# Performance work log

Hardware: AMD Instinct MI355X
Metric: run time of the kernel (lower is better)

## Reference

```python
import jax, jax.numpy as jnp
import numpy as np

# Search geometry (matches init_kwargs)
WS, WT, PS, K, STRIDE0 = 9, 1, 7, 10, 4
SEARCH_INPUT = "noisy"
ALPHA = 0.5
CRIT = "l2"


def _extract_patches(vid, ti, hi, wi):
    """vid: [T,H,W,C]; ti/hi/wi int32 with shape [...] (patch top-left corners).
    Returns [..., PS*PS*C] with clamped (edge-replicated) boundary handling."""
    T, H, W, C = vid.shape
    dy = jnp.arange(PS)
    dx = jnp.arange(PS)
    hh = jnp.clip(hi[..., None, None] + dy[:, None], 0, H - 1)  # [...,PS,1]
    ww = jnp.clip(wi[..., None, None] + dx[None, :], 0, W - 1)  # [...,1,PS]
    p = vid[ti[..., None, None], hh, ww]  # [...,PS,PS,C]
    return p.reshape(p.shape[:-3] + (PS * PS * C,))


def _nls(vid, fflow, bflow):
    """NonLocalSearch: vid [T,H,W,C], flows [T,H,W,2] (channel 0 = x/w, 1 = y/h).
    Returns (topk_dists [nq,K], inds = (ti,hi,wi,tk,hk,wk))."""
    T, H, W, C = vid.shape
    nH, nW = H // STRIDE0, W // STRIDE0
    ti, hi, wi = jnp.meshgrid(jnp.arange(T), jnp.arange(nH) * STRIDE0,
                              jnp.arange(nW) * STRIDE0, indexing="ij")
    ti, hi, wi = ti.reshape(-1), hi.reshape(-1), wi.reshape(-1)  # [nq]
    q = _extract_patches(vid, ti, hi, wi)  # [nq, PS*PS*C]

    ff = fflow[ti, hi, wi]  # [nq,2] flow to frame t+1
    bf = bflow[ti, hi, wi]  # [nq,2] flow to frame t-1
    zero = jnp.zeros_like(ff)
    flow_dt = jnp.stack([bf, zero, ff], axis=1)  # [nq, 2*WT+1, 2] for dt=-1,0,+1
    dts = jnp.arange(-WT, WT + 1)
    tj = jnp.clip(ti[:, None] + dts[None, :], 0, T - 1)  # [nq, 2*WT+1]
    bh = jnp.clip(hi[:, None] + jnp.round(flow_dt[..., 1]).astype(jnp.int32), 0, H - 1)
    bw = jnp.clip(wi[:, None] + jnp.round(flow_dt[..., 0]).astype(jnp.int32), 0, W - 1)

    # Candidate schedule: (dt_index, oy, ox) for all (2*WT+1)*WS*WS candidates.
    r = WS // 2
    oy, ox = np.meshgrid(np.arange(-r, r + 1), np.arange(-r, r + 1), indexing="ij")
    nt = 2 * WT + 1
    specs = np.stack([np.repeat(np.arange(nt), WS * WS),
                      np.tile(oy.ravel(), nt),
                      np.tile(ox.ravel(), nt)], axis=1).astype(np.int32)  # [S,3]

    def step(_, spec):
        di, sy, sx = spec[0], spec[1], spec[2]
        tjc = tj[:, di]
        hj = jnp.clip(bh[:, di] + sy, 0, H - 1)
        wj = jnp.clip(bw[:, di] + sx, 0, W - 1)
        cp = _extract_patches(vid, tjc, hj, wj)  # [nq,D]
        d = jnp.sum((q - cp) ** 2, axis=-1)  # L2 patch distance, [nq]
        return None, (d, tjc, hj, wj)

    _, (dists, tjs, hjs, wjs) = jax.lax.scan(step, None, jnp.asarray(specs))
    # dists: [S, nq] -> top-K smallest per query
    negd, idx = jax.lax.top_k(-dists.T, K)  # [nq,K]
    tk = jnp.take_along_axis(tjs.T, idx, axis=1)
    hk = jnp.take_along_axis(hjs.T, idx, axis=1)
    wk = jnp.take_along_axis(wjs.T, idx, axis=1)
    return -negd, (ti, hi, wi, tk, hk, wk)


def _refine(vid, inds):
    """RefineSearch with wr=1,kr=1: recompute L2 patch distances at given inds."""
    ti, hi, wi, tk, hk, wk = inds
    q = _extract_patches(vid, ti, hi, wi)          # [nq, D]
    cp = _extract_patches(vid, tk, hk, wk)         # [nq, K, D]
    return jnp.sum((q[:, None, :] - cp) ** 2, axis=-1)  # [nq, K]


def setup_inputs() -> dict:
    key = jax.random.key(0)
    k1, k2, k3, k4 = jax.random.split(key, 4)
    B, T, C, H, W = 1, 5, 3, 384, 384
    noisy = jax.random.normal(k1, (B, T, C, H, W), dtype=jnp.float32)
    deno = jax.random.normal(k2, (B, T, C, H, W), dtype=jnp.float32)
    fflow = jax.random.normal(k3, (B, T, 2, H, W), dtype=jnp.float32)
    bflow = jax.random.normal(k4, (B, T, 2, H, W), dtype=jnp.float32)
    return {"noisy": noisy, "deno": deno, "fflow": fflow, "bflow": bflow}


def reference(noisy, deno, fflow, bflow):
    def per_video(nv, dv, ff, bf):
        nv_t = jnp.transpose(nv, (0, 2, 3, 1))  # [T,H,W,C]
        dv_t = jnp.transpose(dv, (0, 2, 3, 1))
        ff_t = jnp.transpose(ff, (0, 2, 3, 1))  # [T,H,W,2]
        bf_t = jnp.transpose(bf, (0, 2, 3, 1))
        if SEARCH_INPUT == "noisy":
            srch = nv_t
        elif SEARCH_INPUT == "deno":
            srch = dv_t
        else:  # interp
            srch = ALPHA * nv_t + (1.0 - ALPHA) * dv_t
        _, inds = _nls(srch, ff_t, bf_t)
        return _refine(nv_t, inds)  # [nq, K]

    dists = jax.vmap(per_video)(noisy, deno, fflow, bflow)  # [B, nq, K]
    if CRIT == "l1":
        return jnp.mean(jnp.sqrt(dists))
    return jnp.mean(dists)
```

## Files before the change

kernel.cpp:

```cpp
#include <hip/hip_runtime.h>

#define TT 5
#define HH 384
#define WW 384
#define CC 3
#define PS_ 7
#define WSR 4
#define NH_ 96
#define NW_ 96
#define NQ_ (TT*NH_*NW_)
#define NCAND 243
#define KK 10

typedef _Float16 h2v __attribute__((ext_vector_type(2)));
union U32H2 { unsigned u; h2v h; };

__global__ __launch_bounds__(256) void nls_kernel(
    const float* __restrict__ vid,
    const float* __restrict__ fflow,
    const float* __restrict__ bflow,
    float* __restrict__ ws)
{
    const int q   = blockIdx.x;
    const int tid = threadIdx.x;
    const int t   = q / (NH_*NW_);
    const int rem = q % (NH_*NW_);
    const int hi  = (rem / NW_) * 4;
    const int wi  = (rem % NW_) * 4;

    __shared__ unsigned reg_lds[2160];
    __shared__ unsigned qp_lds[84];
    __shared__ float dist[256];

    const float ffx = fflow[((t*2+0)*HH + hi)*WW + wi];
    const float ffy = fflow[((t*2+1)*HH + hi)*WW + wi];
    const float bfx = bflow[((t*2+0)*HH + hi)*WW + wi];
    const float bfy = bflow[((t*2+1)*HH + hi)*WW + wi];

    const int tj0 = (t-1 < 0) ? 0 : (t-1);
    const int tj2 = (t+1 > TT-1) ? (TT-1) : (t+1);
    const int bh0 = min(max(hi + (int)rintf(bfy), 0), HH-1);
    const int bw0 = min(max(wi + (int)rintf(bfx), 0), WW-1);
    const int bh2 = min(max(hi + (int)rintf(ffy), 0), HH-1);
    const int bw2 = min(max(wi + (int)rintf(ffx), 0), WW-1);
    const int rm0 = max(bh0-WSR, 0), cm0 = max(bw0-WSR, 0);
    const int rm1 = max(hi -WSR, 0), cm1 = max(wi -WSR, 0);
    const int rm2 = max(bh2-WSR, 0), cm2 = max(bw2-WSR, 0);

    for (int i = tid; i < 2160; i += 256) {
        int d  = i / 720;
        int rr = i % 720;
        int c  = rr / 240;
        int r2 = rr % 240;
        int r  = r2 >> 4;
        int k  = r2 & 15;
        int tjd = (d==0) ? tj0 : ((d==1) ? t   : tj2);
        int rm  = (d==0) ? rm0 : ((d==1) ? rm1 : rm2);
        int cm  = (d==0) ? cm0 : ((d==1) ? cm1 : cm2);
        int col0 = (k < 8) ? (2*k) : (2*(k-8)+1);
        int row  = min(rm + r, HH-1);
        const float* vrow = vid + (size_t)((tjd*CC + c)*HH + row)*WW;
        float v0 = vrow[min(cm+col0,   WW-1)];
        float v1 = vrow[min(cm+col0+1, WW-1)];
        U32H2 u; u.h.x = (_Float16)v0; u.h.y = (_Float16)v1;
        reg_lds[i] = u.u;
    }
    if (tid < 84) {
        int c  = tid / 28;
        int rr = tid % 28;
        int dy = rr >> 2;
        int k  = rr & 3;
        int row = min(hi+dy, HH-1);
        const float* vrow = vid + (size_t)((t*CC + c)*HH + row)*WW;
        float v0 = vrow[min(wi + 2*k, WW-1)];
        float v1 = (k==3) ? 0.0f : vrow[min(wi + 2*k + 1, WW-1)];
        U32H2 u; u.h.x = (_Float16)v0; u.h.y = (_Float16)v1;
        qp_lds[tid] = u.u;
    }
    __syncthreads();

    float acc = 0.0f;
    if (tid < NCAND) {
        int di = tid / 81;
        int s  = tid % 81;
        int sy = s / 9 - WSR;
        int sx = s % 9 - WSR;
        int bhd = (di==0) ? bh0 : ((di==1) ? hi : bh2);
        int bwd = (di==0) ? bw0 : ((di==1) ? wi : bw2);
        int rm  = (di==0) ? rm0 : ((di==1) ? rm1 : rm2);
        int cm  = (di==0) ? cm0 : ((di==1) ? cm1 : cm2);
        int hj = min(max(bhd + sy, 0), HH-1);
        int wj = min(max(bwd + sx, 0), WW-1);
        int roff = hj - rm;
        int woff = wj - cm;
        int par  = woff & 1;
        int cb   = (woff >> 1) + (par << 3);
        const unsigned* rbase = reg_lds + ((di*3*15 + roff)*16 + cb);
        #pragma unroll
        for (int c = 0; c < CC; c++) {
            const unsigned* rc = rbase + c*240;
            #pragma unroll
            for (int dy = 0; dy < PS_; dy++) {
                #pragma unroll
                for (int k = 0; k < 4; k++) {
                    U32H2 a, b, d;
                    a.u = rc[dy*16 + k];
                    b.u = qp_lds[c*28 + dy*4 + k];
                    d.h = a.h - b.h;
                    if (k == 3) d.u &= 0x0000FFFFu;
#if defined(__has_builtin) && __has_builtin(__builtin_amdgcn_fdot2)
                    acc = __builtin_amdgcn_fdot2(d.h, d.h, acc, false);
#else
                    acc += (float)d.h.x*(float)d.h.x + (float)d.h.y*(float)d.h.y;
#endif
                }
            }
        }
    }
    dist[tid] = (tid < NCAND) ? acc : __int_as_float(0x7f800000);
    __syncthreads();

    if (tid < 64) {
        float sumk = 0.0f;
        #pragma unroll 1
        for (int k = 0; k < KK; k++) {
            unsigned key = 0xFFFFFFFFu;
            #pragma unroll
            for (int j = 0; j < 4; j++) {
                int slot = tid + j*64;
                unsigned b = __float_as_uint(dist[slot]);
                unsigned pk = (b & 0xFFFFFF00u) | (unsigned)slot;
                key = min(key, pk);
            }
            #pragma unroll
            for (int ofs = 1; ofs < 64; ofs <<= 1)
                key = min(key, (unsigned)__shfl_xor((int)key, ofs, 64));
            int slot = (int)(key & 0xFFu);
            sumk += dist[slot];
            if (tid == 0) dist[slot] = __int_as_float(0x7f800000);
        }
        if (tid == 0) ws[q] = sumk;
    }
}

__global__ __launch_bounds__(1024) void reduce_kernel(
    const float* __restrict__ ws, float* __restrict__ out)
{
    __shared__ float sdata[1024];
    float s = 0.0f;
    for (int i = threadIdx.x; i < NQ_; i += 1024) s += ws[i];
    sdata[threadIdx.x] = s;
    __syncthreads();
    for (int ofs = 512; ofs > 0; ofs >>= 1) {
        if ((int)threadIdx.x < ofs) sdata[threadIdx.x] += sdata[threadIdx.x + ofs];
        __syncthreads();
    }
    if (threadIdx.x == 0) out[0] = sdata[0] * (1.0f / (float)(NQ_ * KK));
}

extern "C" void kernel_launch(void* const* d_in, const int* in_sizes, int n_in,
                              void* d_out, int out_size, void* d_ws, size_t ws_size,
                              hipStream_t stream) {
    const float* noisy = (const float*)d_in[0];
    const float* fflow = (const float*)d_in[2];
    const float* bflow = (const float*)d_in[3];
    float* ws  = (float*)d_ws;
    float* out = (float*)d_out;

    nls_kernel<<<NQ_, 256, 0, stream>>>(noisy, fflow, bflow, ws);
    reduce_kernel<<<1, 1024, 0, stream>>>(ws, out);
}
```

Baseline: 285.6 us.

## Expand L2 distance into norms minus dot product with precomputed row sums

Rewrites each candidate distance as |q|^2 + |p|^2 - 2 q·p. The query norm is computed once and the candidate patch norms come from sliding-window row sums built in shared memory, so the inner loop becomes a single fdot2 per packed pair. The region load now uses float2 global reads into a padded (stride-17) LDS layout, and the odd-offset shifted copy is built in shared memory afterwards. It also uses round-toward-zero packed fp16 conversion and keeps the top-k keys in registers instead of rereading LDS each iteration. The expansion adds cancellation error in fp16/fp32, which is only partly contained by clamping negative distances to zero, and it adds one more barrier phase.

```diff
diff --git a/kernel.cpp b/kernel.cpp
--- a/kernel.cpp
+++ b/kernel.cpp
@@ -12,8 +12,24 @@
 #define NCAND 243
 #define KK 10
 
+#define RST 17
+#define RCH (15*RST)
+#define RDI (3*RCH)
+#define RSZ (3*RDI)
+
 typedef _Float16 h2v __attribute__((ext_vector_type(2)));
-union U32H2 { unsigned u; h2v h; };
+typedef __fp16   f2v __attribute__((ext_vector_type(2)));
+union U32H2 { unsigned u; h2v h; f2v f; };
+
+static __device__ __forceinline__ unsigned pack_f16(float a, float b) {
+    U32H2 u;
+#if defined(__has_builtin) && __has_builtin(__builtin_amdgcn_cvt_pkrtz)
+    u.f = __builtin_amdgcn_cvt_pkrtz(a, b);
+#else
+    u.h.x = (_Float16)a; u.h.y = (_Float16)b;
+#endif
+    return u.u;
+}
 
 __global__ __launch_bounds__(256) void nls_kernel(
     const float* __restrict__ vid,
@@ -28,116 +44,164 @@
     const int hi  = (rem / NW_) * 4;
     const int wi  = (rem % NW_) * 4;
 
-    __shared__ unsigned reg_lds[2160];
+    __shared__ unsigned reg_lds[RSZ];
     __shared__ unsigned qp_lds[84];
-    __shared__ float dist[256];
+    __shared__ float    rowsum_lds[3*15*12];
+    __shared__ float    dist[256];
+    __shared__ float    qn_lds;
 
     const float ffx = fflow[((t*2+0)*HH + hi)*WW + wi];
     const float ffy = fflow[((t*2+1)*HH + hi)*WW + wi];
     const float bfx = bflow[((t*2+0)*HH + hi)*WW + wi];
     const float bfy = bflow[((t*2+1)*HH + hi)*WW + wi];
 
-    const int tj0 = (t-1 < 0) ? 0 : (t-1);
-    const int tj2 = (t+1 > TT-1) ? (TT-1) : (t+1);
+    const int tj0 = max(t-1, 0);
+    const int tj2 = min(t+1, TT-1);
     const int bh0 = min(max(hi + (int)rintf(bfy), 0), HH-1);
     const int bw0 = min(max(wi + (int)rintf(bfx), 0), WW-1);
     const int bh2 = min(max(hi + (int)rintf(ffy), 0), HH-1);
     const int bw2 = min(max(wi + (int)rintf(ffx), 0), WW-1);
-    const int rm0 = max(bh0-WSR, 0), cm0 = max(bw0-WSR, 0);
-    const int rm1 = max(hi -WSR, 0), cm1 = max(wi -WSR, 0);
-    const int rm2 = max(bh2-WSR, 0), cm2 = max(bw2-WSR, 0);
-
-    for (int i = tid; i < 2160; i += 256) {
-        int d  = i / 720;
-        int rr = i % 720;
-        int c  = rr / 240;
-        int r2 = rr % 240;
-        int r  = r2 >> 4;
-        int k  = r2 & 15;
-        int tjd = (d==0) ? tj0 : ((d==1) ? t   : tj2);
-        int rm  = (d==0) ? rm0 : ((d==1) ? rm1 : rm2);
-        int cm  = (d==0) ? cm0 : ((d==1) ? cm1 : cm2);
-        int col0 = (k < 8) ? (2*k) : (2*(k-8)+1);
-        int row  = min(rm + r, HH-1);
-        const float* vrow = vid + (size_t)((tjd*CC + c)*HH + row)*WW;
-        float v0 = vrow[min(cm+col0,   WW-1)];
-        float v1 = vrow[min(cm+col0+1, WW-1)];
-        U32H2 u; u.h.x = (_Float16)v0; u.h.y = (_Float16)v1;
-        reg_lds[i] = u.u;
+    const int rm0 = max(bh0-WSR,0), rm1 = max(hi-WSR,0), rm2 = max(bh2-WSR,0);
+    const int cm0 = max(bw0-WSR,0), cm1 = max(wi-WSR,0), cm2 = max(bw2-WSR,0);
+    const int ca0 = cm0 & ~1,       ca1 = cm1 & ~1,      ca2 = cm2 & ~1;
+
+    for (int i = tid; i < 1215; i += 256) {
+        int row = i / 9, j = i - row*9;
+        int di  = row / 45; int r45 = row - di*45;
+        int c   = r45 / 15; int r   = r45 - c*15;
+        int tjd = (di==0)?tj0:((di==1)?t  :tj2);
+        int rm  = (di==0)?rm0:((di==1)?rm1:rm2);
+        int ca  = (di==0)?ca0:((di==1)?ca1:ca2);
+        int rr  = min(rm + r, HH-1);
+        const float* vrow = vid + (size_t)((tjd*CC+c)*HH + rr)*WW;
+        float v0, v1;
+        if (ca < 367) {
+            float2 p = *(const float2*)(vrow + ca + 2*j);
+            v0 = p.x; v1 = p.y;
+        } else {
+            v0 = vrow[min(ca+2*j,   WW-1)];
+            v1 = vrow[min(ca+2*j+1, WW-1)];
+        }
+        reg_lds[row*RST + j] = pack_f16(v0, v1);
     }
     if (tid < 84) {
         int c  = tid / 28;
-        int rr = tid % 28;
+        int rr = tid - c*28;
         int dy = rr >> 2;
         int k  = rr & 3;
         int row = min(hi+dy, HH-1);
         const float* vrow = vid + (size_t)((t*CC + c)*HH + row)*WW;
         float v0 = vrow[min(wi + 2*k, WW-1)];
         float v1 = (k==3) ? 0.0f : vrow[min(wi + 2*k + 1, WW-1)];
-        U32H2 u; u.h.x = (_Float16)v0; u.h.y = (_Float16)v1;
-        qp_lds[tid] = u.u;
-    }
-    __syncthreads();
-
-    float acc = 0.0f;
+        qp_lds[tid] = pack_f16(v0, v1);
+    }
+    __syncthreads();
+
+    if (tid < 192) {
+        for (int i = tid; i < 1080; i += 192) {
+            int row = i >> 3, jj = i & 7;
+            int base = row*RST;
+            unsigned a0 = reg_lds[base + jj];
+            unsigned a1 = reg_lds[base + jj + 1];
+            reg_lds[base + 9 + jj] = (a0 >> 16) | (a1 << 16);
+        }
+    } else if (tid < 237) {
+        int rid = tid - 192;
+        int di = rid / 15, r = rid - di*15;
+        float s[16];
+        #pragma unroll
+        for (int x = 0; x < 16; x++) s[x] = 0.f;
+        #pragma unroll
+        for (int c = 0; c < 3; c++) {
+            int base = (di*3+c)*RCH + r*RST;
+            #pragma unroll
+            for (int j = 0; j < 8; j++) {
+                U32H2 u; u.u = reg_lds[base + j];
+                float lo = (float)u.h.x, hh = (float)u.h.y;
+                s[2*j]   = fmaf(lo, lo, s[2*j]);
+                s[2*j+1] = fmaf(hh, hh, s[2*j+1]);
+            }
+        }
+        float rs = s[0]+s[1]+s[2]+s[3]+s[4]+s[5]+s[6];
+        int ob = (di*15 + r)*12;
+        rowsum_lds[ob] = rs;
+        #pragma unroll
+        for (int x0 = 1; x0 < 10; x0++) {
+            rs += s[x0+6] - s[x0-1];
+            rowsum_lds[ob + x0] = rs;
+        }
+    } else if (tid == 248) {
+        float qn = 0.f;
+        #pragma unroll
+        for (int k = 0; k < 84; k++) {
+            U32H2 u; u.u = qp_lds[k];
+            qn = __builtin_amdgcn_fdot2(u.h, u.h, qn, false);
+        }
+        qn_lds = qn;
+    }
+    __syncthreads();
+
+    float dmy = __int_as_float(0x7f800000);
     if (tid < NCAND) {
-        int di = tid / 81;
-        int s  = tid % 81;
-        int sy = s / 9 - WSR;
-        int sx = s % 9 - WSR;
-        int bhd = (di==0) ? bh0 : ((di==1) ? hi : bh2);
-        int bwd = (di==0) ? bw0 : ((di==1) ? wi : bw2);
-        int rm  = (di==0) ? rm0 : ((di==1) ? rm1 : rm2);
-        int cm  = (di==0) ? cm0 : ((di==1) ? cm1 : cm2);
+        int di  = tid / 81; int s81 = tid - di*81;
+        int syq = s81 / 9;  int sx  = s81 - syq*9 - WSR;
+        int sy  = syq - WSR;
+        int bhd = (di==0)?bh0:((di==1)?hi :bh2);
+        int bwd = (di==0)?bw0:((di==1)?wi :bw2);
+        int rm  = (di==0)?rm0:((di==1)?rm1:rm2);
+        int ca  = (di==0)?ca0:((di==1)?ca1:ca2);
         int hj = min(max(bhd + sy, 0), HH-1);
         int wj = min(max(bwd + sx, 0), WW-1);
         int roff = hj - rm;
-        int woff = wj - cm;
-        int par  = woff & 1;
-        int cb   = (woff >> 1) + (par << 3);
-        const unsigned* rbase = reg_lds + ((di*3*15 + roff)*16 + cb);
-        #pragma unroll
-        for (int c = 0; c < CC; c++) {
-            const unsigned* rc = rbase + c*240;
+        int wof  = wj - ca;
+        int cb   = (wof >> 1) + (wof & 1)*9;
+        float dot = 0.f;
+        #pragma unroll
+        for (int c = 0; c < 3; c++) {
+            const unsigned* rc = reg_lds + (di*3+c)*RCH + roff*RST + cb;
+            const unsigned* qc = qp_lds + c*28;
             #pragma unroll
-            for (int dy = 0; dy < PS_; dy++) {
+            for (int dy = 0; dy < 7; dy++) {
                 #pragma unroll
                 for (int k = 0; k < 4; k++) {
-                    U32H2 a, b, d;
-                    a.u = rc[dy*16 + k];
-                    b.u = qp_lds[c*28 + dy*4 + k];
-                    d.h = a.h - b.h;
-                    if (k == 3) d.u &= 0x0000FFFFu;
-#if defined(__has_builtin) && __has_builtin(__builtin_amdgcn_fdot2)
-                    acc = __builtin_amdgcn_fdot2(d.h, d.h, acc, false);
-#else
-                    acc += (float)d.h.x*(float)d.h.x + (float)d.h.y*(float)d.h.y;
-#endif
+                    U32H2 a, b;
+                    a.u = rc[dy*RST + k];
+                    b.u = qc[dy*4 + k];
+                    dot = __builtin_amdgcn_fdot2(a.h, b.h, dot, false);
                 }
             }
         }
-    }
-    dist[tid] = (tid < NCAND) ? acc : __int_as_float(0x7f800000);
+        float c2 = 0.f;
+        int rb = (di*15 + roff)*12 + wof;
+        #pragma unroll
+        for (int i = 0; i < 7; i++) c2 += rowsum_lds[rb + i*12];
+        dmy = fmaxf(fmaf(-2.f, dot, qn_lds + c2), 0.f);
+    }
+    dist[tid] = dmy;
     __syncthreads();
 
     if (tid < 64) {
-        float sumk = 0.0f;
+        float v0 = dist[tid], v1 = dist[tid+64], v2 = dist[tid+128], v3 = dist[tid+192];
+        unsigned k0 = (__float_as_uint(v0) & 0xFFFFFF00u) | (unsigned)tid;
+        unsigned k1 = (__float_as_uint(v1) & 0xFFFFFF00u) | (unsigned)(tid+64);
+        unsigned k2 = (__float_as_uint(v2) & 0xFFFFFF00u) | (unsigned)(tid+128);
+        unsigned k3 = (__float_as_uint(v3) & 0xFFFFFF00u) | (unsigned)(tid+192);
+        float sumk = 0.f;
         #pragma unroll 1
         for (int k = 0; k < KK; k++) {
-            unsigned key = 0xFFFFFFFFu;
-            #pragma unroll
-            for (int j = 0; j < 4; j++) {
-                int slot = tid + j*64;
-                unsigned b = __float_as_uint(dist[slot]);
-                unsigned pk = (b & 0xFFFFFF00u) | (unsigned)slot;
-                key = min(key, pk);
-            }
+            unsigned m = min(min(k0,k1), min(k2,k3));
             #pragma unroll
             for (int ofs = 1; ofs < 64; ofs <<= 1)
-                key = min(key, (unsigned)__shfl_xor((int)key, ofs, 64));
-            int slot = (int)(key & 0xFFu);
-            sumk += dist[slot];
-            if (tid == 0) dist[slot] = __int_as_float(0x7f800000);
+                m = min(m, (unsigned)__shfl_xor((int)m, ofs, 64));
+            int slot = (int)(m & 0xFFu);
+            int lw = slot & 63, jw = slot >> 6;
+            float vj = (jw==0)?v0:((jw==1)?v1:((jw==2)?v2:v3));
+            sumk += __shfl(vj, lw, 64);
+            bool me = (tid == lw);
+            if (me && jw==0) k0 = 0xFFFFFFFFu;
+            if (me && jw==1) k1 = 0xFFFFFFFFu;
+            if (me && jw==2) k2 = 0xFFFFFFFFu;
+            if (me && jw==3) k3 = 0xFFFFFFFFu;
         }
         if (tid == 0) ws[q] = sumk;
     }
```

New measurement: 314.9 us. 1.1x slower.
